# Optimization experiments

Measured on AMD Instinct MI355X. Metric: run time of the kernel, lower is better.

The kernel has to match this reference:

```python
import jax, jax.numpy as jnp
import numpy as np

SEQ, B = 512, 2048
H, OUT = 512, 1
IN = 32  # linearIn input_size; x feature dim = IN - OUT = 31


def setup_inputs() -> dict:
    key = jax.random.key(0)
    ks = jax.random.split(key, 12)
    u = lambda k, shape, lim: jax.random.uniform(k, shape, jnp.float32, -lim, lim)
    lim_in = 1.0 / np.sqrt(IN)
    lim_h = 1.0 / np.sqrt(H)
    return {
        "x": jax.random.normal(ks[0], (SEQ, B, IN - OUT), jnp.float32),
        # initial states (torch eval path uses randn*0.1)
        "h0": jax.random.normal(ks[1], (B, H), jnp.float32) * 0.1,
        "c0": jax.random.normal(ks[2], (B, H), jnp.float32) * 0.1,
        "y0": jax.random.normal(ks[3], (B, OUT), jnp.float32) * 0.1,
        # linearIn
        "W_in": u(ks[4], (H, IN), lim_in),
        "b_in": u(ks[5], (H,), lim_in),
        # single-layer LSTM (gate order i, f, g, o as in PyTorch)
        "W_ih": u(ks[6], (4 * H, H), lim_h),
        "W_hh": u(ks[7], (4 * H, H), lim_h),
        "b_ih": u(ks[8], (4 * H,), lim_h),
        "b_hh": u(ks[9], (4 * H,), lim_h),
        # linearOut
        "W_out": u(ks[10], (OUT, H), lim_h),
        "b_out": u(ks[11], (OUT,), lim_h),
    }


def reference(x, h0, c0, y0, W_in, b_in, W_ih, W_hh, b_ih, b_hh, W_out, b_out):
    b_gate = b_ih + b_hh

    def step(carry, xt):
        h, c, y = carry  # [B,H], [B,H], [B,OUT]
        inp = jnp.concatenate([xt, y], axis=-1)          # [B, IN]
        x0 = jax.nn.relu(inp @ W_in.T + b_in)            # [B, H]
        gates = x0 @ W_ih.T + h @ W_hh.T + b_gate        # [B, 4H]
        i, f, g, o = jnp.split(gates, 4, axis=-1)
        c = jax.nn.sigmoid(f) * c + jax.nn.sigmoid(i) * jnp.tanh(g)
        h = jax.nn.sigmoid(o) * jnp.tanh(c)
        y = h @ W_out.T + b_out                          # [B, OUT]
        return (h, c, y), y

    _, ys = jax.lax.scan(step, (h0, c0, y0), x)
    return ys  # [SEQ, B, OUT]
```

## Files before the change

### kernel.cpp

```cpp
#include <hip/hip_runtime.h>
#include <hip/hip_bf16.h>
#include <stdint.h>

#define SEQ   512
#define BATCH 2048
#define HID   512
#define XF    31

typedef __bf16 bf16_t;
typedef bf16_t bf16x8 __attribute__((ext_vector_type(8)));
typedef bf16_t bf16x4 __attribute__((ext_vector_type(4)));
typedef float  f32x4  __attribute__((ext_vector_type(4)));

__device__ __forceinline__ void gload16(const void* g, void* lds) {
    __builtin_amdgcn_global_load_lds(
        (const __attribute__((address_space(1))) void*)g,
        (__attribute__((address_space(3))) void*)lds,
        16, 0, 0);
}

__device__ __forceinline__ float sigmoid_f(float x) {
    return 1.f / (1.f + __expf(-x));
}
__device__ __forceinline__ float tanh_f(float x) {
    float e = __expf(2.f * x);
    return 1.f - 2.f / (e + 1.f);
}

__global__ void prep_w(const float* __restrict__ W_ih, const float* __restrict__ W_hh,
                       bf16_t* __restrict__ Wcat) {
    const int j = blockIdx.x;
    for (int k = threadIdx.x; k < 1024; k += 256) {
        float v = (k < 512) ? W_ih[(size_t)j * 512 + k]
                            : W_hh[(size_t)j * 512 + (k - 512)];
        Wcat[(size_t)j * 1024 + k] = (bf16_t)v;
    }
}

__global__ void prep_state(const float* __restrict__ h0, const float* __restrict__ c0,
                           bf16_t* __restrict__ H0, float* __restrict__ Cbuf,
                           float* __restrict__ out_all) {
    const int b = blockIdx.x;
    for (int d = threadIdx.x; d < 512; d += 256) {
        H0[(size_t)b * 512 + d]   = (bf16_t)h0[(size_t)b * 512 + d];
        Cbuf[(size_t)b * 512 + d] = c0[(size_t)b * 512 + d];
        out_all[(size_t)b * 512 + d] = 0.f;
    }
}

__global__ void prep_bias(const float* __restrict__ b_ih, const float* __restrict__ b_hh,
                          float* __restrict__ bg) {
    int j = blockIdx.x * 256 + threadIdx.x;
    bg[j] = b_ih[j] + b_hh[j];
}

__global__ void prep_wb(const float* __restrict__ W_in,
                        bf16_t* __restrict__ Wbh, bf16_t* __restrict__ Wbl) {
    int idx = blockIdx.x * 256 + threadIdx.x;
    float v = W_in[idx];
    bf16_t h = (bf16_t)v;
    Wbh[idx] = h;
    Wbl[idx] = (bf16_t)(v - (float)h);
}

__global__ __launch_bounds__(512, 1) void step_fused(
    const float*  __restrict__ x_t,
    const float*  __restrict__ yprev,
    const bf16_t* __restrict__ Wbh,
    const bf16_t* __restrict__ Wbl,
    const float*  __restrict__ b_in,
    const bf16_t* __restrict__ Hin,
    bf16_t*       __restrict__ Hout,
    float*        __restrict__ Cbuf,
    const bf16_t* __restrict__ Wcat,
    const float*  __restrict__ b_gate,
    const float*  __restrict__ W_out,
    const float*  __restrict__ b_out,
    float*        __restrict__ yout)
{
    __shared__ __align__(16) char smem[163840];
    float (*Gs0)[128] = (float (*)[128])smem;
    float (*Gs1)[128] = (float (*)[128])(smem + 65536);

    const int tid  = threadIdx.x;
    const int lane = tid & 63;
    const int wid  = tid >> 6;
    const int wm   = wid >> 2;
    const int wn   = (wid >> 1) & 1;
    const int wk   = wid & 1;

    const int bid  = blockIdx.x;
    const int xcd  = bid & 7;
    const int slot = bid >> 3;
    const int mb   = (xcd >> 1) * 4 + (slot & 3);
    const int nb   = (xcd & 1) * 8 + (slot >> 2);

    const int r  = lane & 15, q = lane >> 4;
    const int lr  = lane >> 3;
    const int lcs = ((lane & 7) ^ lr) * 8;
    const int kob = (((wk << 2) + q) ^ (r & 7)) * 16;

    bf16x8 xh[8], xl[8];
#pragma unroll
    for (int g = 0; g < 8; ++g) {
        const int row = mb * 128 + g * 16 + r;
        const float* bp = x_t + (size_t)row * XF + q * 8;
        float tmp[8];
#pragma unroll
        for (int j = 0; j < 7; ++j) tmp[j] = bp[j];
        const float* p7 = (q == 3) ? (yprev + row) : (bp + 7);
        tmp[7] = *p7;
#pragma unroll
        for (int j = 0; j < 8; ++j) {
            bf16_t h = (bf16_t)tmp[j];
            xh[g][j] = h;
            xl[g][j] = (bf16_t)(tmp[j] - (float)h);
        }
    }

    f32x4 acc[4][4];
#pragma unroll
    for (int mi = 0; mi < 4; ++mi)
#pragma unroll
        for (int ni = 0; ni < 4; ++ni) {
            f32x4 z = {0.f, 0.f, 0.f, 0.f};
            acc[mi][ni] = z;
        }

    auto stageAB = [&](int dst, int kt) {
        const int k0 = (kt - 8) * 64;
#pragma unroll
        for (int iss = 0; iss < 2; ++iss) {
            const int r0 = wid * 16 + iss * 8;
            gload16(Hin + (size_t)(mb * 128 + r0 + lr) * 512 + k0 + lcs,
                    smem + (size_t)dst * 16384 + r0 * 128);
        }
#pragma unroll
        for (int iss = 0; iss < 2; ++iss) {
            const int r0   = wid * 16 + iss * 8;
            const int nloc = r0 + lr;
            const int j    = (nloc >> 5) * 512 + nb * 32 + (nloc & 31);
            gload16(Wcat + (size_t)j * 1024 + kt * 64 + lcs,
                    smem + 65536 + (size_t)dst * 16384 + r0 * 128);
        }
    };
    auto stageB2 = [&](int dst, int kt) {
#pragma unroll
        for (int iss = 0; iss < 2; ++iss) {
            const int r0   = wid * 16 + iss * 8;
            const int nloc = r0 + lr;
            const int j    = (nloc >> 5) * 512 + nb * 32 + (nloc & 31);
            gload16(Wcat + (size_t)j * 1024 + kt * 64 + lcs,
                    smem + 131072 + (size_t)dst * 16384 + r0 * 128);
        }
    };

    stageAB(0, 8);
    stageAB(1, 9);
#pragma unroll
    for (int kt = 8; kt < 16; ++kt) {
        if (kt + 2 < 16) stageAB((kt + 2) & 3, kt + 2);
        if (kt < 14) {
            asm volatile("s_waitcnt vmcnt(8)" ::: "memory");
        } else if (kt == 14) {
            asm volatile("s_waitcnt vmcnt(4)" ::: "memory");
        } else {
            asm volatile("s_waitcnt vmcnt(0)" ::: "memory");
        }
        __builtin_amdgcn_s_barrier();
        __builtin_amdgcn_sched_barrier(0);

        const int cur = kt & 3;
        const char* Ab = smem + (size_t)cur * 16384;
        const char* Bb = smem + 65536 + (size_t)cur * 16384;
        bf16x8 af[4], bfr[4];
#pragma unroll
        for (int mi = 0; mi < 4; ++mi)
            af[mi] = *(const bf16x8*)(Ab + (wm * 64 + mi * 16 + r) * 128 + kob);
#pragma unroll
        for (int ni = 0; ni < 4; ++ni)
            bfr[ni] = *(const bf16x8*)(Bb + (wn * 64 + ni * 16 + r) * 128 + kob);
#pragma unroll
        for (int mi = 0; mi < 4; ++mi)
#pragma unroll
            for (int ni = 0; ni < 4; ++ni)
                acc[mi][ni] = __builtin_amdgcn_mfma_f32_16x16x32_bf16(
                    af[mi], bfr[ni], acc[mi][ni], 0, 0, 0);
    }

    __syncthreads();

    bf16x8 wfh[4], wfl[4];
    float4 bi4[4];
#pragma unroll
    for (int u = 0; u < 4; ++u) {
        const int dt = wid * 4 + u;
        const size_t wo_ = (size_t)(dt * 16 + r) * 32 + q * 8;
        wfh[u] = *(const bf16x8*)&Wbh[wo_];
        wfl[u] = *(const bf16x8*)&Wbl[wo_];
        bi4[u] = *(const float4*)&b_in[dt * 16 + q * 4];
    }
    stageB2(0, 0);
    stageB2(1, 1);

#pragma unroll
    for (int u = 0; u < 4; ++u) {
        const int dt = wid * 4 + u;
#pragma unroll
        for (int g = 0; g < 8; ++g) {
            f32x4 pa = {0.f, 0.f, 0.f, 0.f};
            pa = __builtin_amdgcn_mfma_f32_16x16x32_bf16(wfh[u], xh[g], pa, 0, 0, 0);
            pa = __builtin_amdgcn_mfma_f32_16x16x32_bf16(wfh[u], xl[g], pa, 0, 0, 0);
            pa = __builtin_amdgcn_mfma_f32_16x16x32_bf16(wfl[u], xh[g], pa, 0, 0, 0);
            bf16x4 hv;
            hv[0] = (bf16_t)fmaxf(pa[0] + bi4[u].x, 0.f);
            hv[1] = (bf16_t)fmaxf(pa[1] + bi4[u].y, 0.f);
            hv[2] = (bf16_t)fmaxf(pa[2] + bi4[u].z, 0.f);
            hv[3] = (bf16_t)fmaxf(pa[3] + bi4[u].w, 0.f);
            const int c  = dt * 2 + (q >> 1);
            const int cs = (c & ~7) | ((c & 7) ^ (r & 7));
            *(bf16x4*)(smem + (size_t)(g * 16 + r) * 1024 + cs * 16 + (q & 1) * 8) = hv;
        }
    }

    __syncthreads();

#pragma unroll
    for (int kt = 0; kt < 8; ++kt) {
        if (kt < 7) {
            asm volatile("s_waitcnt vmcnt(2)" ::: "memory");
        } else {
            asm volatile("s_waitcnt vmcnt(0)" ::: "memory");
        }
        __builtin_amdgcn_s_barrier();
        __builtin_amdgcn_sched_barrier(0);

        const char* Bb = smem + 131072 + (size_t)(kt & 1) * 16384;
        bf16x8 af[4], bfr[4];
#pragma unroll
        for (int mi = 0; mi < 4; ++mi)
            af[mi] = *(const bf16x8*)(smem + (size_t)(wm * 64 + mi * 16 + r) * 1024
                                      + kt * 128 + kob);
#pragma unroll
        for (int ni = 0; ni < 4; ++ni)
            bfr[ni] = *(const bf16x8*)(Bb + (wn * 64 + ni * 16 + r) * 128 + kob);
#pragma unroll
        for (int mi = 0; mi < 4; ++mi)
#pragma unroll
            for (int ni = 0; ni < 4; ++ni)
                acc[mi][ni] = __builtin_amdgcn_mfma_f32_16x16x32_bf16(
                    af[mi], bfr[ni], acc[mi][ni], 0, 0, 0);
        __builtin_amdgcn_s_barrier();
        if (kt + 2 < 8) stageB2(kt & 1, kt + 2);
    }

    const int row    = tid >> 2;
    const int dq     = (tid & 3) * 8;
    const int b_glob = mb * 128 + row;

    float cv[8], wo[8];
    *(float4*)&cv[0] = *(const float4*)&Cbuf[(size_t)b_glob * 512 + nb * 32 + dq];
    *(float4*)&cv[4] = *(const float4*)&Cbuf[(size_t)b_glob * 512 + nb * 32 + dq + 4];
    *(float4*)&wo[0] = *(const float4*)&W_out[nb * 32 + dq];
    *(float4*)&wo[4] = *(const float4*)&W_out[nb * 32 + dq + 4];
    const float bo = b_out[0];

    __syncthreads();

    {
        float (*G)[128] = wk ? Gs1 : Gs0;
#pragma unroll
        for (int mi = 0; mi < 4; ++mi)
#pragma unroll
            for (int ni = 0; ni < 4; ++ni)
#pragma unroll
                for (int rr = 0; rr < 4; ++rr) {
                    const int gr = wm * 64 + mi * 16 + q * 4 + rr;
                    const int gc = wn * 64 + ni * 16 + r;
                    G[gr][gc ^ ((gr & 7) << 2)] = acc[mi][ni][rr];
                }
    }
    __syncthreads();

    {
        const int sx = (row & 7) << 2;
        float cnew[8];
        bf16_t hv[8];
        float yp = 0.f;
#pragma unroll
        for (int ii = 0; ii < 8; ++ii) {
            const int dl     = dq + ii;
            const int d_glob = nb * 32 + dl;
            const int c0x = (dl)      ^ sx;
            const int c1x = (32 + dl) ^ sx;
            const int c2x = (64 + dl) ^ sx;
            const int c3x = (96 + dl) ^ sx;
            float gi = Gs0[row][c0x] + Gs1[row][c0x] + b_gate[d_glob];
            float gf = Gs0[row][c1x] + Gs1[row][c1x] + b_gate[512  + d_glob];
            float gg = Gs0[row][c2x] + Gs1[row][c2x] + b_gate[1024 + d_glob];
            float go = Gs0[row][c3x] + Gs1[row][c3x] + b_gate[1536 + d_glob];
            float is = sigmoid_f(gi);
            float fs = sigmoid_f(gf);
            float os = sigmoid_f(go);
            float gt = tanh_f(gg);
            float c_new = fs * cv[ii] + is * gt;
            float hval  = os * tanh_f(c_new);
            cnew[ii] = c_new;
            hv[ii]   = (bf16_t)hval;
            yp += hval * wo[ii];
        }
        const size_t base = (size_t)b_glob * 512 + nb * 32 + dq;
        *(float4*)&Cbuf[base]     = *(const float4*)&cnew[0];
        *(float4*)&Cbuf[base + 4] = *(const float4*)&cnew[4];
        *(bf16x8*)&Hout[base]     = *(const bf16x8*)&hv[0];

        yp += __shfl_xor(yp, 1);
        yp += __shfl_xor(yp, 2);
        if ((tid & 3) == 0)
            atomicAdd(&yout[b_glob], yp + ((nb == 0) ? bo : 0.f));
    }
}

extern "C" void kernel_launch(void* const* d_in, const int* in_sizes, int n_in,
                              void* d_out, int out_size, void* d_ws, size_t ws_size,
                              hipStream_t stream) {
    const float* x     = (const float*)d_in[0];
    const float* h0    = (const float*)d_in[1];
    const float* c0    = (const float*)d_in[2];
    const float* y0    = (const float*)d_in[3];
    const float* W_in  = (const float*)d_in[4];
    const float* b_in  = (const float*)d_in[5];
    const float* W_ih  = (const float*)d_in[6];
    const float* W_hh  = (const float*)d_in[7];
    const float* b_ih  = (const float*)d_in[8];
    const float* b_hh  = (const float*)d_in[9];
    const float* W_out = (const float*)d_in[10];
    const float* b_out = (const float*)d_in[11];
    float* out = (float*)d_out;

    char* ws = (char*)d_ws;
    bf16_t* Wcat  = (bf16_t*)(ws);
    bf16_t* Hb0   = (bf16_t*)(ws + (4u << 20));
    bf16_t* Hb1   = (bf16_t*)(ws + (6u << 20));
    float*  Cbuf  = (float*)(ws + (8u << 20));
    float*  bgate = (float*)(ws + (12u << 20));
    bf16_t* Wbh   = (bf16_t*)(ws + (12u << 20) + (16u << 10));
    bf16_t* Wbl   = (bf16_t*)(ws + (12u << 20) + (64u << 10));
    bf16_t* Hb[2] = { Hb0, Hb1 };

    prep_w    <<<2048, 256, 0, stream>>>(W_ih, W_hh, Wcat);
    prep_state<<<2048, 256, 0, stream>>>(h0, c0, Hb[0], Cbuf, out);
    prep_bias <<<8,    256, 0, stream>>>(b_ih, b_hh, bgate);
    prep_wb   <<<64,   256, 0, stream>>>(W_in, Wbh, Wbl);

    for (int t = 0; t < SEQ; ++t) {
        const float* yprev = (t == 0) ? y0 : (out + (size_t)(t - 1) * BATCH);
        step_fused<<<256, 512, 0, stream>>>(
            x + (size_t)t * BATCH * XF, yprev, Wbh, Wbl, b_in,
            Hb[t & 1], Hb[(t + 1) & 1], Cbuf, Wcat, bgate, W_out, b_out,
            out + (size_t)t * BATCH);
    }
    (void)in_sizes; (void)n_in; (void)out_size; (void)ws_size;
}
```

Before: 11.33 ms.

## Replace per-timestep launches with persistent kernel and per-row-group spin barriers

New measurement: 29.43 ms. 160% more time.

```diff
diff --git a/kernel.cpp b/kernel.cpp
--- a/kernel.cpp
+++ b/kernel.cpp
@@ -37,15 +37,15 @@
     }
 }
 
-__global__ void prep_state(const float* __restrict__ h0, const float* __restrict__ c0,
-                           bf16_t* __restrict__ H0, float* __restrict__ Cbuf,
-                           float* __restrict__ out_all) {
+__global__ void prep_state(const float* __restrict__ h0,
+                           bf16_t* __restrict__ H0, float* __restrict__ out_all,
+                           unsigned* __restrict__ bar) {
     const int b = blockIdx.x;
     for (int d = threadIdx.x; d < 512; d += 256) {
-        H0[(size_t)b * 512 + d]   = (bf16_t)h0[(size_t)b * 512 + d];
-        Cbuf[(size_t)b * 512 + d] = c0[(size_t)b * 512 + d];
+        H0[(size_t)b * 512 + d] = (bf16_t)h0[(size_t)b * 512 + d];
         out_all[(size_t)b * 512 + d] = 0.f;
     }
+    if (blockIdx.x == 0 && threadIdx.x < 16) bar[threadIdx.x] = 0u;
 }
 
 __global__ void prep_bias(const float* __restrict__ b_ih, const float* __restrict__ b_hh,
@@ -63,20 +63,21 @@
     Wbl[idx] = (bf16_t)(v - (float)h);
 }
 
-__global__ __launch_bounds__(512, 1) void step_fused(
-    const float*  __restrict__ x_t,
-    const float*  __restrict__ yprev,
+__global__ __launch_bounds__(512, 1) void step_persist(
+    const float*  __restrict__ x_all,
+    const float*  __restrict__ y0,
     const bf16_t* __restrict__ Wbh,
     const bf16_t* __restrict__ Wbl,
     const float*  __restrict__ b_in,
-    const bf16_t* __restrict__ Hin,
-    bf16_t*       __restrict__ Hout,
-    float*        __restrict__ Cbuf,
+    const float*  __restrict__ c0,
+    bf16_t*       __restrict__ Hb0,
+    bf16_t*       __restrict__ Hb1,
     const bf16_t* __restrict__ Wcat,
     const float*  __restrict__ b_gate,
     const float*  __restrict__ W_out,
     const float*  __restrict__ b_out,
-    float*        __restrict__ yout)
+    float*        __restrict__ out,
+    unsigned*     __restrict__ bar)
 {
     __shared__ __align__(16) char smem[163840];
     float (*Gs0)[128] = (float (*)[128])smem;
@@ -100,96 +101,6 @@
     const int lcs = ((lane & 7) ^ lr) * 8;
     const int kob = (((wk << 2) + q) ^ (r & 7)) * 16;
 
-    bf16x8 xh[8], xl[8];
-#pragma unroll
-    for (int g = 0; g < 8; ++g) {
-        const int row = mb * 128 + g * 16 + r;
-        const float* bp = x_t + (size_t)row * XF + q * 8;
-        float tmp[8];
-#pragma unroll
-        for (int j = 0; j < 7; ++j) tmp[j] = bp[j];
-        const float* p7 = (q == 3) ? (yprev + row) : (bp + 7);
-        tmp[7] = *p7;
-#pragma unroll
-        for (int j = 0; j < 8; ++j) {
-            bf16_t h = (bf16_t)tmp[j];
-            xh[g][j] = h;
-            xl[g][j] = (bf16_t)(tmp[j] - (float)h);
-        }
-    }
-
-    f32x4 acc[4][4];
-#pragma unroll
-    for (int mi = 0; mi < 4; ++mi)
-#pragma unroll
-        for (int ni = 0; ni < 4; ++ni) {
-            f32x4 z = {0.f, 0.f, 0.f, 0.f};
-            acc[mi][ni] = z;
-        }
-
-    auto stageAB = [&](int dst, int kt) {
-        const int k0 = (kt - 8) * 64;
-#pragma unroll
-        for (int iss = 0; iss < 2; ++iss) {
-            const int r0 = wid * 16 + iss * 8;
-            gload16(Hin + (size_t)(mb * 128 + r0 + lr) * 512 + k0 + lcs,
-                    smem + (size_t)dst * 16384 + r0 * 128);
-        }
-#pragma unroll
-        for (int iss = 0; iss < 2; ++iss) {
-            const int r0   = wid * 16 + iss * 8;
-            const int nloc = r0 + lr;
-            const int j    = (nloc >> 5) * 512 + nb * 32 + (nloc & 31);
-            gload16(Wcat + (size_t)j * 1024 + kt * 64 + lcs,
-                    smem + 65536 + (size_t)dst * 16384 + r0 * 128);
-        }
-    };
-    auto stageB2 = [&](int dst, int kt) {
-#pragma unroll
-        for (int iss = 0; iss < 2; ++iss) {
-            const int r0   = wid * 16 + iss * 8;
-            const int nloc = r0 + lr;
-            const int j    = (nloc >> 5) * 512 + nb * 32 + (nloc & 31);
-            gload16(Wcat + (size_t)j * 1024 + kt * 64 + lcs,
-                    smem + 131072 + (size_t)dst * 16384 + r0 * 128);
-        }
-    };
-
-    stageAB(0, 8);
-    stageAB(1, 9);
-#pragma unroll
-    for (int kt = 8; kt < 16; ++kt) {
-        if (kt + 2 < 16) stageAB((kt + 2) & 3, kt + 2);
-        if (kt < 14) {
-            asm volatile("s_waitcnt vmcnt(8)" ::: "memory");
-        } else if (kt == 14) {
-            asm volatile("s_waitcnt vmcnt(4)" ::: "memory");
-        } else {
-            asm volatile("s_waitcnt vmcnt(0)" ::: "memory");
-        }
-        __builtin_amdgcn_s_barrier();
-        __builtin_amdgcn_sched_barrier(0);
-
-        const int cur = kt & 3;
-        const char* Ab = smem + (size_t)cur * 16384;
-        const char* Bb = smem + 65536 + (size_t)cur * 16384;
-        bf16x8 af[4], bfr[4];
-#pragma unroll
-        for (int mi = 0; mi < 4; ++mi)
-            af[mi] = *(const bf16x8*)(Ab + (wm * 64 + mi * 16 + r) * 128 + kob);
-#pragma unroll
-        for (int ni = 0; ni < 4; ++ni)
-            bfr[ni] = *(const bf16x8*)(Bb + (wn * 64 + ni * 16 + r) * 128 + kob);
-#pragma unroll
-        for (int mi = 0; mi < 4; ++mi)
-#pragma unroll
-            for (int ni = 0; ni < 4; ++ni)
-                acc[mi][ni] = __builtin_amdgcn_mfma_f32_16x16x32_bf16(
-                    af[mi], bfr[ni], acc[mi][ni], 0, 0, 0);
-    }
-
-    __syncthreads();
-
     bf16x8 wfh[4], wfl[4];
     float4 bi4[4];
 #pragma unroll
@@ -200,125 +111,239 @@
         wfl[u] = *(const bf16x8*)&Wbl[wo_];
         bi4[u] = *(const float4*)&b_in[dt * 16 + q * 4];
     }
-    stageB2(0, 0);
-    stageB2(1, 1);
-
-#pragma unroll
-    for (int u = 0; u < 4; ++u) {
-        const int dt = wid * 4 + u;
-#pragma unroll
-        for (int g = 0; g < 8; ++g) {
-            f32x4 pa = {0.f, 0.f, 0.f, 0.f};
-            pa = __builtin_amdgcn_mfma_f32_16x16x32_bf16(wfh[u], xh[g], pa, 0, 0, 0);
-            pa = __builtin_amdgcn_mfma_f32_16x16x32_bf16(wfh[u], xl[g], pa, 0, 0, 0);
-            pa = __builtin_amdgcn_mfma_f32_16x16x32_bf16(wfl[u], xh[g], pa, 0, 0, 0);
-            bf16x4 hv;
-            hv[0] = (bf16_t)fmaxf(pa[0] + bi4[u].x, 0.f);
-            hv[1] = (bf16_t)fmaxf(pa[1] + bi4[u].y, 0.f);
-            hv[2] = (bf16_t)fmaxf(pa[2] + bi4[u].z, 0.f);
-            hv[3] = (bf16_t)fmaxf(pa[3] + bi4[u].w, 0.f);
-            const int c  = dt * 2 + (q >> 1);
-            const int cs = (c & ~7) | ((c & 7) ^ (r & 7));
-            *(bf16x4*)(smem + (size_t)(g * 16 + r) * 1024 + cs * 16 + (q & 1) * 8) = hv;
-        }
-    }
-
-    __syncthreads();
-
-#pragma unroll
-    for (int kt = 0; kt < 8; ++kt) {
-        if (kt < 7) {
-            asm volatile("s_waitcnt vmcnt(2)" ::: "memory");
-        } else {
-            asm volatile("s_waitcnt vmcnt(0)" ::: "memory");
-        }
-        __builtin_amdgcn_s_barrier();
-        __builtin_amdgcn_sched_barrier(0);
-
-        const char* Bb = smem + 131072 + (size_t)(kt & 1) * 16384;
-        bf16x8 af[4], bfr[4];
-#pragma unroll
-        for (int mi = 0; mi < 4; ++mi)
-            af[mi] = *(const bf16x8*)(smem + (size_t)(wm * 64 + mi * 16 + r) * 1024
-                                      + kt * 128 + kob);
-#pragma unroll
-        for (int ni = 0; ni < 4; ++ni)
-            bfr[ni] = *(const bf16x8*)(Bb + (wn * 64 + ni * 16 + r) * 128 + kob);
-#pragma unroll
-        for (int mi = 0; mi < 4; ++mi)
-#pragma unroll
-            for (int ni = 0; ni < 4; ++ni)
-                acc[mi][ni] = __builtin_amdgcn_mfma_f32_16x16x32_bf16(
-                    af[mi], bfr[ni], acc[mi][ni], 0, 0, 0);
-        __builtin_amdgcn_s_barrier();
-        if (kt + 2 < 8) stageB2(kt & 1, kt + 2);
-    }
-
-    const int row    = tid >> 2;
-    const int dq     = (tid & 3) * 8;
-    const int b_glob = mb * 128 + row;
-
+    const int row_e   = tid >> 2;
+    const int dq      = (tid & 3) * 8;
+    const int b_glob  = mb * 128 + row_e;
     float cv[8], wo[8];
-    *(float4*)&cv[0] = *(const float4*)&Cbuf[(size_t)b_glob * 512 + nb * 32 + dq];
-    *(float4*)&cv[4] = *(const float4*)&Cbuf[(size_t)b_glob * 512 + nb * 32 + dq + 4];
+    *(float4*)&cv[0] = *(const float4*)&c0[(size_t)b_glob * 512 + nb * 32 + dq];
+    *(float4*)&cv[4] = *(const float4*)&c0[(size_t)b_glob * 512 + nb * 32 + dq + 4];
     *(float4*)&wo[0] = *(const float4*)&W_out[nb * 32 + dq];
     *(float4*)&wo[4] = *(const float4*)&W_out[nb * 32 + dq + 4];
     const float bo = b_out[0];
-
-    __syncthreads();
-
-    {
-        float (*G)[128] = wk ? Gs1 : Gs0;
+    int bailed = 0;
+
+    const bf16_t* Hin = Hb0;
+#define STAGE_AB(dst, kt)                                                     \
+    {                                                                          \
+        const int k0 = ((kt) - 8) * 64;                                        \
+        _Pragma("unroll")                                                      \
+        for (int iss = 0; iss < 2; ++iss) {                                    \
+            const int r0 = wid * 16 + iss * 8;                                 \
+            gload16(Hin + (size_t)(mb * 128 + r0 + lr) * 512 + k0 + lcs,       \
+                    smem + (size_t)(dst) * 16384 + r0 * 128);                  \
+        }                                                                      \
+        _Pragma("unroll")                                                      \
+        for (int iss = 0; iss < 2; ++iss) {                                    \
+            const int r0   = wid * 16 + iss * 8;                               \
+            const int nloc = r0 + lr;                                          \
+            const int j    = (nloc >> 5) * 512 + nb * 32 + (nloc & 31);        \
+            gload16(Wcat + (size_t)j * 1024 + (kt) * 64 + lcs,                 \
+                    smem + 65536 + (size_t)(dst) * 16384 + r0 * 128);          \
+        }                                                                      \
+    }
+#define STAGE_B2(dst, kt)                                                     \
+    {                                                                          \
+        _Pragma("unroll")                                                      \
+        for (int iss = 0; iss < 2; ++iss) {                                    \
+            const int r0   = wid * 16 + iss * 8;                               \
+            const int nloc = r0 + lr;                                          \
+            const int j    = (nloc >> 5) * 512 + nb * 32 + (nloc & 31);        \
+            gload16(Wcat + (size_t)j * 1024 + (kt) * 64 + lcs,                 \
+                    smem + 131072 + (size_t)(dst) * 16384 + r0 * 128);         \
+        }                                                                      \
+    }
+
+#pragma unroll 1
+    for (int t = 0; t < SEQ; ++t) {
+        const float* x_t   = x_all + (size_t)t * BATCH * XF;
+        const float* yprev = (t == 0) ? y0 : (out + (size_t)(t - 1) * BATCH);
+        float*       yout  = out + (size_t)t * BATCH;
+        Hin                = (t & 1) ? Hb1 : Hb0;
+        bf16_t*      Hout  = (t & 1) ? Hb0 : Hb1;
+
+        bf16x8 xh[8], xl[8];
+#pragma unroll
+        for (int g = 0; g < 8; ++g) {
+            const int row = mb * 128 + g * 16 + r;
+            const float* bp = x_t + (size_t)row * XF + q * 8;
+            float tmp[8];
+#pragma unroll
+            for (int j = 0; j < 7; ++j) tmp[j] = bp[j];
+            const float* p7 = (q == 3) ? (yprev + row) : (bp + 7);
+            tmp[7] = *p7;
+#pragma unroll
+            for (int j = 0; j < 8; ++j) {
+                bf16_t h = (bf16_t)tmp[j];
+                xh[g][j] = h;
+                xl[g][j] = (bf16_t)(tmp[j] - (float)h);
+            }
+        }
+
+        f32x4 acc[4][4];
 #pragma unroll
         for (int mi = 0; mi < 4; ++mi)
 #pragma unroll
+            for (int ni = 0; ni < 4; ++ni) {
+                f32x4 z = {0.f, 0.f, 0.f, 0.f};
+                acc[mi][ni] = z;
+            }
+
+        STAGE_AB(0, 8);
+        STAGE_AB(1, 9);
+#pragma unroll
+        for (int kt = 8; kt < 16; ++kt) {
+            if (kt + 2 < 16) STAGE_AB((kt + 2) & 3, kt + 2);
+            if (kt < 14) {
+                asm volatile("s_waitcnt vmcnt(8)" ::: "memory");
+            } else if (kt == 14) {
+                asm volatile("s_waitcnt vmcnt(4)" ::: "memory");
+            } else {
+                asm volatile("s_waitcnt vmcnt(0)" ::: "memory");
+            }
+            __builtin_amdgcn_s_barrier();
+            __builtin_amdgcn_sched_barrier(0);
+
+            const int cur = kt & 3;
+            const char* Ab = smem + (size_t)cur * 16384;
+            const char* Bb = smem + 65536 + (size_t)cur * 16384;
+            bf16x8 af[4], bfr[4];
+#pragma unroll
+            for (int mi = 0; mi < 4; ++mi)
+                af[mi] = *(const bf16x8*)(Ab + (wm * 64 + mi * 16 + r) * 128 + kob);
+#pragma unroll
             for (int ni = 0; ni < 4; ++ni)
-#pragma unroll
-                for (int rr = 0; rr < 4; ++rr) {
-                    const int gr = wm * 64 + mi * 16 + q * 4 + rr;
-                    const int gc = wn * 64 + ni * 16 + r;
-                    G[gr][gc ^ ((gr & 7) << 2)] = acc[mi][ni][rr];
+                bfr[ni] = *(const bf16x8*)(Bb + (wn * 64 + ni * 16 + r) * 128 + kob);
+#pragma unroll
+            for (int mi = 0; mi < 4; ++mi)
+#pragma unroll
+                for (int ni = 0; ni < 4; ++ni)
+                    acc[mi][ni] = __builtin_amdgcn_mfma_f32_16x16x32_bf16(
+                        af[mi], bfr[ni], acc[mi][ni], 0, 0, 0);
+        }
+
+        __syncthreads();
+
+        STAGE_B2(0, 0);
+        STAGE_B2(1, 1);
+#pragma unroll
+        for (int u = 0; u < 4; ++u) {
+            const int dt = wid * 4 + u;
+#pragma unroll
+            for (int g = 0; g < 8; ++g) {
+                f32x4 pa = {0.f, 0.f, 0.f, 0.f};
+                pa = __builtin_amdgcn_mfma_f32_16x16x32_bf16(wfh[u], xh[g], pa, 0, 0, 0);
+                pa = __builtin_amdgcn_mfma_f32_16x16x32_bf16(wfh[u], xl[g], pa, 0, 0, 0);
+                pa = __builtin_amdgcn_mfma_f32_16x16x32_bf16(wfl[u], xh[g], pa, 0, 0, 0);
+                bf16x4 hv;
+                hv[0] = (bf16_t)fmaxf(pa[0] + bi4[u].x, 0.f);
+                hv[1] = (bf16_t)fmaxf(pa[1] + bi4[u].y, 0.f);
+                hv[2] = (bf16_t)fmaxf(pa[2] + bi4[u].z, 0.f);
+                hv[3] = (bf16_t)fmaxf(pa[3] + bi4[u].w, 0.f);
+                const int c  = dt * 2 + (q >> 1);
+                const int cs = (c & ~7) | ((c & 7) ^ (r & 7));
+                *(bf16x4*)(smem + (size_t)(g * 16 + r) * 1024 + cs * 16 + (q & 1) * 8) = hv;
+            }
+        }
+
+        __syncthreads();
+
+#pragma unroll
+        for (int kt = 0; kt < 8; ++kt) {
+            if (kt < 7) {
+                asm volatile("s_waitcnt vmcnt(2)" ::: "memory");
+            } else {
+                asm volatile("s_waitcnt vmcnt(0)" ::: "memory");
+            }
+            __builtin_amdgcn_s_barrier();
+            __builtin_amdgcn_sched_barrier(0);
+
+            const char* Bb = smem + 131072 + (size_t)(kt & 1) * 16384;
+            bf16x8 af[4], bfr[4];
+#pragma unroll
+            for (int mi = 0; mi < 4; ++mi)
+                af[mi] = *(const bf16x8*)(smem + (size_t)(wm * 64 + mi * 16 + r) * 1024
+                                          + kt * 128 + kob);
+#pragma unroll
+            for (int ni = 0; ni < 4; ++ni)
+                bfr[ni] = *(const bf16x8*)(Bb + (wn * 64 + ni * 16 + r) * 128 + kob);
+#pragma unroll
+            for (int mi = 0; mi < 4; ++mi)
+#pragma unroll
+                for (int ni = 0; ni < 4; ++ni)
+                    acc[mi][ni] = __builtin_amdgcn_mfma_f32_16x16x32_bf16(
+                        af[mi], bfr[ni], acc[mi][ni], 0, 0, 0);
+            __builtin_amdgcn_s_barrier();
+            if (kt + 2 < 8) STAGE_B2(kt & 1, kt + 2);
+        }
+
+        __syncthreads();
+        {
+            float (*G)[128] = wk ? Gs1 : Gs0;
+#pragma unroll
+            for (int mi = 0; mi < 4; ++mi)
+#pragma unroll
+                for (int ni = 0; ni < 4; ++ni)
+#pragma unroll
+                    for (int rr = 0; rr < 4; ++rr) {
+                        const int gr = wm * 64 + mi * 16 + q * 4 + rr;
+                        const int gc = wn * 64 + ni * 16 + r;
+                        G[gr][gc ^ ((gr & 7) << 2)] = acc[mi][ni][rr];
+                    }
+        }
+        __syncthreads();
+        {
+            const int sx = (row_e & 7) << 2;
+            bf16_t hv[8];
+            float yp = 0.f;
+#pragma unroll
+            for (int ii = 0; ii < 8; ++ii) {
+                const int dl     = dq + ii;
+                const int d_glob = nb * 32 + dl;
+                const int c0x = (dl)      ^ sx;
+                const int c1x = (32 + dl) ^ sx;
+                const int c2x = (64 + dl) ^ sx;
+                const int c3x = (96 + dl) ^ sx;
+                float gi = Gs0[row_e][c0x] + Gs1[row_e][c0x] + b_gate[d_glob];
+                float gf = Gs0[row_e][c1x] + Gs1[row_e][c1x] + b_gate[512  + d_glob];
+                float gg = Gs0[row_e][c2x] + Gs1[row_e][c2x] + b_gate[1024 + d_glob];
+                float go = Gs0[row_e][c3x] + Gs1[row_e][c3x] + b_gate[1536 + d_glob];
+                float is = sigmoid_f(gi);
+                float fs = sigmoid_f(gf);
+                float os = sigmoid_f(go);
+                float gt = tanh_f(gg);
+                float c_new = fs * cv[ii] + is * gt;
+                float hval  = os * tanh_f(c_new);
+                cv[ii] = c_new;
+                hv[ii] = (bf16_t)hval;
+                yp += hval * wo[ii];
+            }
+            *(bf16x8*)&Hout[(size_t)b_glob * 512 + nb * 32 + dq] = *(const bf16x8*)&hv[0];
+
+            yp += __shfl_xor(yp, 1);
+            yp += __shfl_xor(yp, 2);
+            if ((tid & 3) == 0)
+                atomicAdd(&yout[b_glob], yp + ((nb == 0) ? bo : 0.f));
+        }
+
+        __syncthreads();
+        if (tid == 0) {
+            __threadfence();
+            atomicAdd(&bar[mb], 1u);
+            if (!bailed) {
+                const unsigned target = 16u * (unsigned)(t + 1);
+                int spins = 0;
+                while (__hip_atomic_load(&bar[mb], __ATOMIC_ACQUIRE,
+                                         __HIP_MEMORY_SCOPE_AGENT) < target) {
+                    __builtin_amdgcn_s_sleep(2);
+                    if (++spins > (1 << 14)) { bailed = 1; break; }
                 }
-    }
-    __syncthreads();
-
-    {
-        const int sx = (row & 7) << 2;
-        float cnew[8];
-        bf16_t hv[8];
-        float yp = 0.f;
-#pragma unroll
-        for (int ii = 0; ii < 8; ++ii) {
-            const int dl     = dq + ii;
-            const int d_glob = nb * 32 + dl;
-            const int c0x = (dl)      ^ sx;
-            const int c1x = (32 + dl) ^ sx;
-            const int c2x = (64 + dl) ^ sx;
-            const int c3x = (96 + dl) ^ sx;
-            float gi = Gs0[row][c0x] + Gs1[row][c0x] + b_gate[d_glob];
-            float gf = Gs0[row][c1x] + Gs1[row][c1x] + b_gate[512  + d_glob];
-            float gg = Gs0[row][c2x] + Gs1[row][c2x] + b_gate[1024 + d_glob];
-            float go = Gs0[row][c3x] + Gs1[row][c3x] + b_gate[1536 + d_glob];
-            float is = sigmoid_f(gi);
-            float fs = sigmoid_f(gf);
-            float os = sigmoid_f(go);
-            float gt = tanh_f(gg);
-            float c_new = fs * cv[ii] + is * gt;
-            float hval  = os * tanh_f(c_new);
-            cnew[ii] = c_new;
-            hv[ii]   = (bf16_t)hval;
-            yp += hval * wo[ii];
-        }
-        const size_t base = (size_t)b_glob * 512 + nb * 32 + dq;
-        *(float4*)&Cbuf[base]     = *(const float4*)&cnew[0];
-        *(float4*)&Cbuf[base + 4] = *(const float4*)&cnew[4];
-        *(bf16x8*)&Hout[base]     = *(const bf16x8*)&hv[0];
-
-        yp += __shfl_xor(yp, 1);
-        yp += __shfl_xor(yp, 2);
-        if ((tid & 3) == 0)
-            atomicAdd(&yout[b_glob], yp + ((nb == 0) ? bo : 0.f));
-    }
+                __builtin_amdgcn_fence(__ATOMIC_ACQUIRE, "agent");
+            }
+        }
+        __syncthreads();
+    }
+#undef STAGE_AB
+#undef STAGE_B2
 }
 
 extern "C" void kernel_launch(void* const* d_in, const int* in_sizes, int n_in,
@@ -339,26 +364,21 @@
     float* out = (float*)d_out;
 
     char* ws = (char*)d_ws;
-    bf16_t* Wcat  = (bf16_t*)(ws);
-    bf16_t* Hb0   = (bf16_t*)(ws + (4u << 20));
-    bf16_t* Hb1   = (bf16_t*)(ws + (6u << 20));
-    float*  Cbuf  = (float*)(ws + (8u << 20));
-    float*  bgate = (float*)(ws + (12u << 20));
-    bf16_t* Wbh   = (bf16_t*)(ws + (12u << 20) + (16u << 10));
-    bf16_t* Wbl   = (bf16_t*)(ws + (12u << 20) + (64u << 10));
-    bf16_t* Hb[2] = { Hb0, Hb1 };
+    bf16_t*   Wcat  = (bf16_t*)(ws);
+    bf16_t*   Hb0   = (bf16_t*)(ws + (4u << 20));
+    bf16_t*   Hb1   = (bf16_t*)(ws + (6u << 20));
+    float*    bgate = (float*)(ws + (8u << 20));
+    bf16_t*   Wbh   = (bf16_t*)(ws + (8u << 20) + (16u << 10));
+    bf16_t*   Wbl   = (bf16_t*)(ws + (8u << 20) + (64u << 10));
+    unsigned* bar   = (unsigned*)(ws + (8u << 20) + (128u << 10));
 
     prep_w    <<<2048, 256, 0, stream>>>(W_ih, W_hh, Wcat);
-    prep_state<<<2048, 256, 0, stream>>>(h0, c0, Hb[0], Cbuf, out);
+    prep_state<<<2048, 256, 0, stream>>>(h0, Hb0, out, bar);
     prep_bias <<<8,    256, 0, stream>>>(b_ih, b_hh, bgate);
     prep_wb   <<<64,   256, 0, stream>>>(W_in, Wbh, Wbl);
 
-    for (int t = 0; t < SEQ; ++t) {
-        const float* yprev = (t == 0) ? y0 : (out + (size_t)(t - 1) * BATCH);
-        step_fused<<<256, 512, 0, stream>>>(
-            x + (size_t)t * BATCH * XF, yprev, Wbh, Wbl, b_in,
-            Hb[t & 1], Hb[(t + 1) & 1], Cbuf, Wcat, bgate, W_out, b_out,
-            out + (size_t)t * BATCH);
-    }
+    step_persist<<<256, 512, 0, stream>>>(
+        x, y0, Wbh, Wbl, b_in, c0, Hb0, Hb1, Wcat, bgate,
+        W_out, b_out, out, bar);
     (void)in_sizes; (void)n_in; (void)out_size; (void)ws_size;
 }
```
